# Optimization experiments

Hardware: AMD Instinct MI355X
Metric: run time of the kernel (lower is better)

The kernel has to match this reference:

```python
import jax, jax.numpy as jnp
import numpy as np

N, E, H, HEADS, L = 10000, 64000, 128, 8, 8
D = H // HEADS
CUTOFF = 5.0
EPS = 1e-5


def _xavier(key, shape):
    lim = float(np.sqrt(6.0 / (shape[0] + shape[1])))
    return jax.random.uniform(key, shape, minval=-lim, maxval=lim, dtype=jnp.float32)


def setup_inputs() -> dict:
    key = jax.random.key(0)
    ks = jax.random.split(key, 20)
    zeros = lambda *s: jnp.zeros(s, jnp.float32)
    return {
        "x": jax.random.normal(ks[0], (N, H), jnp.float32),
        "vec": 0.1 * jax.random.normal(ks[1], (N, L, H), jnp.float32),
        "f_ij": jax.random.normal(ks[2], (E, H), jnp.float32),
        "d_ij": jax.random.normal(ks[3], (E, L), jnp.float32),
        "r_ij": jax.random.uniform(ks[4], (E,), jnp.float32, 0.0, CUTOFF),
        "edge_index": jax.random.randint(ks[5], (2, E), 0, N),
        "ln_g": jnp.ones((H,), jnp.float32), "ln_b": zeros(H),
        "vln_w": jnp.ones((H,), jnp.float32),
        "W_vec": _xavier(ks[6], (H, 3 * H)),
        "W_q": _xavier(ks[7], (H, H)), "b_q": zeros(H),
        "W_k": _xavier(ks[8], (H, H)), "b_k": zeros(H),
        "W_v": _xavier(ks[9], (H, H)), "b_v": zeros(H),
        "W_dk": _xavier(ks[10], (H, H)), "b_dk": zeros(H),
        "W_dv": _xavier(ks[11], (H, H)), "b_dv": zeros(H),
        "W_s": _xavier(ks[12], (H, 2 * H)), "b_s": zeros(2 * H),
        "W_f": _xavier(ks[13], (H, H)), "b_f": zeros(H),
        "W_src": _xavier(ks[14], (H, H)),
        "W_trg": _xavier(ks[15], (H, H)),
        "W_o": _xavier(ks[16], (H, 3 * H)), "b_o": zeros(3 * H),
    }


def _layernorm(x, g, b):
    mu = jnp.mean(x, -1, keepdims=True)
    var = jnp.mean((x - mu) ** 2, -1, keepdims=True)
    return (x - mu) * jax.lax.rsqrt(var + EPS) * g + b


def _cutoff(r):
    # CosineCutoff: 0.5*(cos(pi*r/cutoff)+1) for r < cutoff
    return 0.5 * (jnp.cos(jnp.pi * r / CUTOFF) + 1.0) * (r < CUTOFF).astype(r.dtype)


def _vec_rejection(v, d):
    # v: [E, L, H], d: [E, L]; remove the component of v along d (per channel)
    proj = jnp.einsum("elh,el->eh", v, d)
    return v - proj[:, None, :] * d[:, :, None]


def reference(x, vec, f_ij, d_ij, r_ij, edge_index, ln_g, ln_b, vln_w, W_vec,
              W_q, b_q, W_k, b_k, W_v, b_v, W_dk, b_dk, W_dv, b_dv,
              W_s, b_s, W_f, b_f, W_src, W_trg, W_o, b_o):
    src, dst = edge_index[0], edge_index[1]  # j (source), i (target)
    x = _layernorm(x, ln_g, ln_b)
    vec = vec * vln_w  # VecLayerNorm with norm_type="none": identity norm * weight

    q = (x @ W_q + b_q).reshape(N, HEADS, D)
    k = (x @ W_k + b_k).reshape(N, HEADS, D)
    v = (x @ W_v + b_v).reshape(N, HEADS, D)
    dk = jax.nn.silu(f_ij @ W_dk + b_dk).reshape(E, HEADS, D)
    dv = jax.nn.silu(f_ij @ W_dv + b_dv).reshape(E, HEADS, D)

    vec1, vec2, vec3 = jnp.split(jnp.einsum("nlh,hk->nlk", vec, W_vec), 3, axis=-1)
    vec_dot = jnp.sum(vec1 * vec2, axis=1)  # [N, H]

    # ---- message (per edge) ----
    attn = jnp.sum(q[dst] * k[src] * dk, axis=-1)          # [E, HEADS]
    attn = jax.nn.silu(attn) * _cutoff(r_ij)[:, None]
    vm = (v[src] * dv * attn[:, :, None]).reshape(E, H)    # [E, H]
    s1, s2 = jnp.split(jax.nn.silu(vm @ W_s + b_s), 2, axis=-1)
    vec_m = vec[src] * s1[:, None, :] + s2[:, None, :] * d_ij[:, :, None]  # [E, L, H]

    # ---- aggregate (scatter-add to target nodes) ----
    x_agg = jax.ops.segment_sum(vm, dst, num_segments=N)       # [N, H]
    vec_agg = jax.ops.segment_sum(vec_m, dst, num_segments=N)  # [N, L, H]

    # ---- edge update ----
    w1 = _vec_rejection(jnp.einsum("elh,hk->elk", vec[dst], W_trg), d_ij)
    w2 = _vec_rejection(jnp.einsum("elh,hk->elk", vec[src], W_src), -d_ij)
    w_dot = jnp.sum(w1 * w2, axis=1)                       # [E, H]
    df_ij = jax.nn.silu(f_ij @ W_f + b_f) * w_dot

    # ---- node update ----
    o1, o2, o3 = jnp.split(x_agg @ W_o + b_o, 3, axis=-1)
    dx = vec_dot * o2 + o3
    dvec = vec3 * o1[:, None, :] + vec_agg
    return dx, dvec, df_ij
```

## Files before the change

### kernel.cpp

```cpp
#include <hip/hip_runtime.h>
#include <hip/hip_bf16.h>
#include <math.h>

#define N_NODES 10000
#define N_EDGES 64000
#define H 128
#define L 8
#define NL (N_NODES * L)

typedef __attribute__((ext_vector_type(4))) float f32x4;
typedef __attribute__((ext_vector_type(8))) __bf16 bf16x8;

__device__ __forceinline__ float silu_f(float x) { return x / (1.f + __expf(-x)); }

__global__ __launch_bounds__(256) void ln_kernel(const float* __restrict__ x,
                                                 const float* __restrict__ g,
                                                 const float* __restrict__ b,
                                                 __bf16* __restrict__ out, int n_nodes) {
  int wave = threadIdx.x >> 6;
  int lane = threadIdx.x & 63;
  int n = blockIdx.x * 4 + wave;
  if (n >= n_nodes) return;
  const float* xr = x + (size_t)n * H;
  float a0 = xr[lane], a1 = xr[lane + 64];
  float s = a0 + a1;
#pragma unroll
  for (int off = 32; off >= 1; off >>= 1) s += __shfl_xor(s, off, 64);
  float mu = s * (1.f / H);
  float d0 = a0 - mu, d1 = a1 - mu;
  float v = d0 * d0 + d1 * d1;
#pragma unroll
  for (int off = 32; off >= 1; off >>= 1) v += __shfl_xor(v, off, 64);
  float rstd = rsqrtf(v * (1.f / H) + 1e-5f);
  __bf16* orow = out + (size_t)n * H;
  orow[lane] = (__bf16)(d0 * rstd * g[lane] + b[lane]);
  orow[lane + 64] = (__bf16)(d1 * rstd * g[lane + 64] + b[lane + 64]);
}

__global__ __launch_bounds__(256) void vecw_kernel(const float* __restrict__ vec,
                                                   const float* __restrict__ w,
                                                   __bf16* __restrict__ out, size_t total8) {
  size_t i = (size_t)blockIdx.x * blockDim.x + threadIdx.x;
  size_t stride = (size_t)gridDim.x * blockDim.x;
  for (; i < total8; i += stride) {
    size_t base = i * 8;
    f32x4 a = *(const f32x4*)(vec + base);
    f32x4 b = *(const f32x4*)(vec + base + 4);
    int c = (int)(base & 127);
    bf16x8 h;
    h[0] = (__bf16)(a[0] * w[c + 0]); h[1] = (__bf16)(a[1] * w[c + 1]);
    h[2] = (__bf16)(a[2] * w[c + 2]); h[3] = (__bf16)(a[3] * w[c + 3]);
    h[4] = (__bf16)(b[0] * w[c + 4]); h[5] = (__bf16)(b[1] * w[c + 5]);
    h[6] = (__bf16)(b[2] * w[c + 6]); h[7] = (__bf16)(b[3] * w[c + 7]);
    *(bf16x8*)(out + base) = h;
  }
}

__global__ __launch_bounds__(256) void f2b_kernel(const float* __restrict__ in,
                                                  __bf16* __restrict__ out, size_t total8) {
  size_t i = (size_t)blockIdx.x * blockDim.x + threadIdx.x;
  size_t stride = (size_t)gridDim.x * blockDim.x;
  for (; i < total8; i += stride) {
    size_t base = i * 8;
    f32x4 a = *(const f32x4*)(in + base);
    f32x4 b = *(const f32x4*)(in + base + 4);
    bf16x8 h;
    h[0] = (__bf16)a[0]; h[1] = (__bf16)a[1]; h[2] = (__bf16)a[2]; h[3] = (__bf16)a[3];
    h[4] = (__bf16)b[0]; h[5] = (__bf16)b[1]; h[6] = (__bf16)b[2]; h[7] = (__bf16)b[3];
    *(bf16x8*)(out + base) = h;
  }
}

__global__ __launch_bounds__(256) void wconv_kernel(
    const float* __restrict__ Wvec, const float* __restrict__ Wq, const float* __restrict__ Wk,
    const float* __restrict__ Wv, const float* __restrict__ Wdk, const float* __restrict__ Wdv,
    const float* __restrict__ Ws, const float* __restrict__ Wtrg, const float* __restrict__ Wsrc,
    const float* __restrict__ Wf, const float* __restrict__ Wo,
    const float* __restrict__ bq, const float* __restrict__ bk, const float* __restrict__ bv,
    const float* __restrict__ bdk, const float* __restrict__ bdv, const float* __restrict__ bf,
    __bf16* __restrict__ Wt, float* __restrict__ bqkv, float* __restrict__ bfm) {
  int bid = blockIdx.x;
  int t = threadIdx.x;
  if (bid >= 256) {
    if (bid == 256) {
      if (t < 128) { bqkv[t] = bq[t]; bqkv[128 + t] = bk[t]; bqkv[256 + t] = bv[t]; }
    } else {
      if (t < 128) { bfm[t] = bdk[t]; bfm[128 + t] = bdv[t]; bfm[256 + t] = bf[t]; }
    }
    return;
  }
  int ct = bid >> 2, kt = bid & 3;
  int gc0 = ct * 32;
  const float* W; int ldw, sc0;
  if      (gc0 < 384)  { W = Wvec; ldw = 384; sc0 = gc0; }
  else if (gc0 < 512)  { W = Wtrg; ldw = 128; sc0 = gc0 - 384; }
  else if (gc0 < 640)  { W = Wsrc; ldw = 128; sc0 = gc0 - 512; }
  else if (gc0 < 768)  { W = Wq;   ldw = 128; sc0 = gc0 - 640; }
  else if (gc0 < 896)  { W = Wk;   ldw = 128; sc0 = gc0 - 768; }
  else if (gc0 < 1024) { W = Wv;   ldw = 128; sc0 = gc0 - 896; }
  else if (gc0 < 1152) { W = Wdk;  ldw = 128; sc0 = gc0 - 1024; }
  else if (gc0 < 1280) { W = Wdv;  ldw = 128; sc0 = gc0 - 1152; }
  else if (gc0 < 1408) { W = Wf;   ldw = 128; sc0 = gc0 - 1280; }
  else if (gc0 < 1664) { W = Ws;   ldw = 256; sc0 = gc0 - 1408; }
  else                 { W = Wo;   ldw = 384; sc0 = gc0 - 1664; }
  __shared__ float tile[32][33];
  int tx = t & 31, ty = t >> 5;
#pragma unroll
  for (int i = 0; i < 4; ++i)
    tile[ty + i * 8][tx] = W[(size_t)(kt * 32 + ty + i * 8) * ldw + sc0 + tx];
  __syncthreads();
#pragma unroll
  for (int i = 0; i < 4; ++i)
    Wt[(size_t)(gc0 + ty + i * 8) * 128 + kt * 32 + tx] = (__bf16)tile[tx][ty + i * 8];
}

__global__ __launch_bounds__(256, 2) void vdot_gemm(const __bf16* __restrict__ A,
                                                    const __bf16* __restrict__ Bt,
                                                    float* __restrict__ vdot) {
  __shared__ __bf16 As[128 * 128];
  const int tid = threadIdx.x;
  const int lane = tid & 63;
  const int wave = tid >> 6;
  const int wm = wave >> 1, wn = wave & 1;
  const int row0 = blockIdx.x * 128;

#pragma unroll
  for (int i = 0; i < 8; ++i) {
    int c = tid + i * 256;
    int row = c >> 4, k8 = c & 15;
    int k8s = k8 ^ (row & 7);
    const __bf16* src = A + (size_t)(row0 + row) * 128 + k8s * 8;
    __builtin_amdgcn_global_load_lds((const __attribute__((address_space(1))) void*)src,
                                     (__attribute__((address_space(3))) void*)(As + c * 8),
                                     16, 0, 0);
  }
  __syncthreads();

  f32x4 pacc[4][4], acc[4][4];
#pragma unroll
  for (int mi = 0; mi < 4; ++mi)
#pragma unroll
    for (int ni = 0; ni < 4; ++ni) {
      pacc[mi][ni] = f32x4{0.f, 0.f, 0.f, 0.f};
      acc[mi][ni] = f32x4{0.f, 0.f, 0.f, 0.f};
    }
#pragma unroll
  for (int ct = 0; ct < 2; ++ct) {
    const __bf16* Bbase =
        Bt + ((size_t)(ct * 128 + wn * 64 + (lane & 15)) << 7) + ((lane >> 4) << 3);
#pragma unroll
    for (int ks = 0; ks < 4; ++ks) {
      bf16x8 b[4];
#pragma unroll
      for (int ni = 0; ni < 4; ++ni) b[ni] = *(const bf16x8*)(Bbase + (ni << 11) + (ks << 5));
      bf16x8 a[4];
#pragma unroll
      for (int mi = 0; mi < 4; ++mi) {
        int row = wm * 64 + mi * 16 + (lane & 15);
        int byte = (row * 256 + ks * 64 + ((lane >> 4) << 4)) ^ ((row & 7) << 4);
        a[mi] = *(const bf16x8*)((const char*)As + byte);
      }
      if (ct == 0) {
#pragma unroll
        for (int mi = 0; mi < 4; ++mi)
#pragma unroll
          for (int ni = 0; ni < 4; ++ni)
            pacc[mi][ni] =
                __builtin_amdgcn_mfma_f32_16x16x32_bf16(a[mi], b[ni], pacc[mi][ni], 0, 0, 0);
      } else {
#pragma unroll
        for (int mi = 0; mi < 4; ++mi)
#pragma unroll
          for (int ni = 0; ni < 4; ++ni)
            acc[mi][ni] =
                __builtin_amdgcn_mfma_f32_16x16x32_bf16(a[mi], b[ni], acc[mi][ni], 0, 0, 0);
      }
    }
  }
#pragma unroll
  for (int mi = 0; mi < 4; ++mi) {
#pragma unroll
    for (int ni = 0; ni < 4; ++ni) {
      float sr = pacc[mi][ni][0] * acc[mi][ni][0] + pacc[mi][ni][1] * acc[mi][ni][1] +
                 pacc[mi][ni][2] * acc[mi][ni][2] + pacc[mi][ni][3] * acc[mi][ni][3];
      sr += __shfl_xor(sr, 16, 64);
      if ((lane & 16) == 0) {
        int node = (row0 >> 3) + wm * 8 + mi * 2 + (lane >> 5);
        int col = wn * 64 + ni * 16 + (lane & 15);
        vdot[(size_t)node * 128 + col] = sr;
      }
    }
  }
}

template <typename CT>
__global__ __launch_bounds__(256, 3) void gemm_v9(const __bf16* __restrict__ A,
                                                  const __bf16* __restrict__ Bt,
                                                  const float* __restrict__ bias,
                                                  CT* __restrict__ C, int M, int nx, int ny,
                                                  int ldc, int act) {
  __shared__ __bf16 As[128 * 128];
  __bf16* Cs = As;
  const int bid = blockIdx.x;
  const int xi = bid & 7;
  const int rem = bid >> 3;
  const int y = rem % ny;
  const int x = (rem / ny) * 8 + xi;
  if (x >= nx) return;
  const int tid = threadIdx.x;
  const int lane = tid & 63;
  const int wave = tid >> 6;
  const int wm = wave >> 1, wn = wave & 1;
  const int row0 = x * 128;

#pragma unroll
  for (int i = 0; i < 8; ++i) {
    int c = tid + i * 256;
    int row = c >> 4, k8 = c & 15;
    int k8s = k8 ^ (row & 7);
    const __bf16* src = A + (size_t)(row0 + row) * 128 + k8s * 8;
    __builtin_amdgcn_global_load_lds((const __attribute__((address_space(1))) void*)src,
                                     (__attribute__((address_space(3))) void*)(As + c * 8),
                                     16, 0, 0);
  }
  __syncthreads();

  const __bf16* Bbase =
      Bt + ((size_t)(y * 128 + wn * 64 + (lane & 15)) << 7) + ((lane >> 4) << 3);
  bf16x8 b[4][4];
#pragma unroll
  for (int ks = 0; ks < 4; ++ks)
#pragma unroll
    for (int ni = 0; ni < 4; ++ni) b[ks][ni] = *(const bf16x8*)(Bbase + (ni << 11) + (ks << 5));

  f32x4 acc[4][4];
#pragma unroll
  for (int mi = 0; mi < 4; ++mi)
#pragma unroll
    for (int ni = 0; ni < 4; ++ni) acc[mi][ni] = f32x4{0.f, 0.f, 0.f, 0.f};

#pragma unroll
  for (int ks = 0; ks < 4; ++ks) {
    bf16x8 a[4];
#pragma unroll
    for (int mi = 0; mi < 4; ++mi) {
      int row = wm * 64 + mi * 16 + (lane & 15);
      int byte = (row * 256 + ks * 64 + ((lane >> 4) << 4)) ^ ((row & 7) << 4);
      a[mi] = *(const bf16x8*)((const char*)As + byte);
    }
#pragma unroll
    for (int mi = 0; mi < 4; ++mi)
#pragma unroll
      for (int ni = 0; ni < 4; ++ni)
        acc[mi][ni] =
            __builtin_amdgcn_mfma_f32_16x16x32_bf16(a[mi], b[ks][ni], acc[mi][ni], 0, 0, 0);
  }

  const int cstore = y * 128;
  if constexpr (sizeof(CT) == 2) {
#pragma unroll
    for (int p = 0; p < 2; ++p) {
      __syncthreads();
      int rl = (wm << 5) | ((lane >> 4) << 2);
#pragma unroll
      for (int q = 0; q < 2; ++q) {
        int mi = 2 * p + q;
#pragma unroll
        for (int ni = 0; ni < 4; ++ni) {
          int col = wn * 64 + ni * 16 + (lane & 15);
          float bv = bias ? bias[cstore + col] : 0.f;
#pragma unroll
          for (int r = 0; r < 4; ++r) {
            float xv = acc[mi][ni][r] + bv;
            if (act) xv = silu_f(xv);
            Cs[(rl + q * 16 + r) * 136 + col] = (__bf16)xv;
          }
        }
      }
      __syncthreads();
#pragma unroll
      for (int rr = 0; rr < 4; ++rr) {
        int row = (tid >> 4) + rr * 16;
        int chunk = tid & 15;
        bf16x8 v = *(const bf16x8*)(Cs + row * 136 + chunk * 8);
        int grow = row0 + (row >> 5) * 64 + (2 * p + ((row >> 4) & 1)) * 16 + (row & 15);
        if (grow < M)
          *(bf16x8*)(C + (size_t)grow * ldc + cstore + chunk * 8) = v;
      }
    }
  } else {
#pragma unroll
    for (int mi = 0; mi < 4; ++mi) {
      int rbase = row0 + wm * 64 + mi * 16 + ((lane >> 4) << 2);
#pragma unroll
      for (int ni = 0; ni < 4; ++ni) {
        int gcol = cstore + wn * 64 + ni * 16 + (lane & 15);
        float bv = bias ? bias[cstore + wn * 64 + ni * 16 + (lane & 15)] : 0.f;
#pragma unroll
        for (int r = 0; r < 4; ++r) {
          int grow = rbase + r;
          if (grow < M) {
            float xv = acc[mi][ni][r] + bv;
            if (act) xv = silu_f(xv);
            C[(size_t)grow * ldc + gcol] = (CT)xv;
          }
        }
      }
    }
  }
}

static inline int swz_grid(int nx, int ny) { return ((nx + 7) / 8) * ny * 8; }

__global__ __launch_bounds__(256) void msg_kernel(const __bf16* __restrict__ qkv,
                                                  const __bf16* __restrict__ fm,
                                                  const float* __restrict__ r_ij,
                                                  const int* __restrict__ ei,
                                                  const int* __restrict__ elist,
                                                  __bf16* __restrict__ vm) {
  int p = blockIdx.x * 2 + (threadIdx.x >> 7);
  int h = threadIdx.x & 127;
  int e = elist[p];
  int src = ei[e], dst = ei[N_EDGES + e];
  float qv = (float)qkv[(size_t)dst * 384 + h];
  float kv = (float)qkv[(size_t)src * 384 + 128 + h];
  float vv = (float)qkv[(size_t)src * 384 + 256 + h];
  float t = qv * kv * (float)fm[(size_t)e * 384 + h];
#pragma unroll
  for (int off = 8; off >= 1; off >>= 1) t += __shfl_xor(t, off, 16);
  float r = r_ij[e];
  float cut = 0.5f * (__cosf(0.6283185307f * r) + 1.f);
  cut = (r < 5.f) ? cut : 0.f;
  float attn = silu_f(t) * cut;
  vm[(size_t)e * H + h] = (__bf16)(vv * (float)fm[(size_t)e * 384 + 128 + h] * attn);
}

__global__ __launch_bounds__(256) void hist_kernel(const int* __restrict__ ei,
                                                   int* __restrict__ cnt) {
  int e = blockIdx.x * 256 + threadIdx.x;
  if (e < N_EDGES) atomicAdd(&cnt[ei[N_EDGES + e]], 1);
}

__global__ __launch_bounds__(1024) void scan_kernel(const int* __restrict__ cnt,
                                                    int* __restrict__ rowptr) {
  __shared__ int wsum[16];
  int t = threadIdx.x;
  int base = t * 10;
  int local[10];
  int s = 0;
#pragma unroll
  for (int i = 0; i < 10; ++i) {
    int v = (base + i < N_NODES) ? cnt[base + i] : 0;
    local[i] = s;
    s += v;
  }
  int lane = t & 63, wave = t >> 6;
  int inc = s;
#pragma unroll
  for (int off = 1; off < 64; off <<= 1) {
    int u = __shfl_up(inc, off, 64);
    if (lane >= off) inc += u;
  }
  if (lane == 63) wsum[wave] = inc;
  __syncthreads();
  if (t == 0) {
    int acc = 0;
#pragma unroll
    for (int w = 0; w < 16; ++w) { int v = wsum[w]; wsum[w] = acc; acc += v; }
  }
  __syncthreads();
  int excl = inc - s + wsum[wave];
#pragma unroll
  for (int i = 0; i < 10; ++i)
    if (base + i <= N_NODES) rowptr[base + i] = excl + local[i];
}

__global__ __launch_bounds__(256) void fill_kernel(const int* __restrict__ ei,
                                                   const int* __restrict__ rowptr,
                                                   int* __restrict__ cursor,
                                                   int* __restrict__ elist) {
  int e = blockIdx.x * 256 + threadIdx.x;
  if (e < N_EDGES) {
    int d = ei[N_EDGES + e];
    int p = atomicAdd(&cursor[d], 1);
    elist[rowptr[d] + p] = e;
  }
}

__global__ __launch_bounds__(256) void node_kernel(const __bf16* __restrict__ vm,
                                                   const __bf16* __restrict__ s,
                                                   const __bf16* __restrict__ vecw,
                                                   const __bf16* __restrict__ big,
                                                   const __bf16* __restrict__ fm,
                                                   const float* __restrict__ d_ij,
                                                   const int* __restrict__ ei,
                                                   const int* __restrict__ rowptr,
                                                   const int* __restrict__ elist,
                                                   __bf16* __restrict__ x_agg,
                                                   float* __restrict__ dvec,
                                                   float* __restrict__ df) {
  int n = blockIdx.x * 2 + (threadIdx.x >> 7);
  int h = threadIdx.x & 127;
  if (n >= N_NODES) return;
  int beg = rowptr[n], end = rowptr[n + 1];

  float vt[L];
  const __bf16* trow = big + (size_t)n * 8 * 384 + 128 + h;
#pragma unroll
  for (int l = 0; l < L; l++) vt[l] = (float)trow[l * 384];

  float ax = 0.f;
  float av[L] = {};
  for (int p = beg; p < end; ++p) {
    int e = elist[p];
    int src = ei[e];
    const float* dd = d_ij + (size_t)e * L;
    float d[L], sd2 = 0.f;
#pragma unroll
    for (int l = 0; l < L; l++) {
      d[l] = dd[l];
      sd2 += d[l] * d[l];
    }
    ax += (float)vm[(size_t)e * H + h];
    float s1 = (float)s[(size_t)e * 256 + h];
    float s2 = (float)s[(size_t)e * 256 + 128 + h];
    const __bf16* vrow = vecw + (size_t)src * L * H + h;
    const __bf16* brow = big + (size_t)src * 8 * 384 + 256 + h;
    float dot = 0.f, p1 = 0.f, p2 = 0.f;
#pragma unroll
    for (int l = 0; l < L; l++) {
      float vw = (float)vrow[l * H];
      av[l] += vw * s1 + s2 * d[l];
      float bb = (float)brow[l * 384];
      dot += vt[l] * bb;
      p1 += vt[l] * d[l];
      p2 += bb * d[l];
    }
    float wdot = dot - p1 * p2 * (2.f - sd2);
    df[(size_t)e * H + h] = (float)fm[(size_t)e * 384 + 256 + h] * wdot;
  }
  x_agg[(size_t)n * H + h] = (__bf16)ax;
  float* drow = dvec + (size_t)n * L * H + h;
#pragma unroll
  for (int l = 0; l < L; l++) drow[l * H] = av[l];
}

__global__ __launch_bounds__(256) void final_kernel(const float* __restrict__ o,
                                                    const float* __restrict__ vdot,
                                                    const __bf16* __restrict__ big,
                                                    float* __restrict__ dx,
                                                    float* __restrict__ dvec, int n_nodes) {
  int n = blockIdx.x * 2 + (threadIdx.x >> 7);
  int h = threadIdx.x & 127;
  if (n >= n_nodes) return;
  float o1 = o[(size_t)n * 384 + h];
  float o2 = o[(size_t)n * 384 + 128 + h];
  float o3 = o[(size_t)n * 384 + 256 + h];
  dx[(size_t)n * H + h] = vdot[(size_t)n * H + h] * o2 + o3;
  float* drow = dvec + (size_t)n * L * H + h;
  const __bf16* v3 = big + (size_t)n * 8 * 384 + h;
#pragma unroll
  for (int l = 0; l < L; l++) drow[l * H] += (float)v3[l * 384] * o1;
}

extern "C" void kernel_launch(void* const* d_in, const int* in_sizes, int n_in, void* d_out,
                              int out_size, void* d_ws, size_t ws_size, hipStream_t stream) {
  const float* x = (const float*)d_in[0];
  const float* vec = (const float*)d_in[1];
  const float* f_ij = (const float*)d_in[2];
  const float* d_ij = (const float*)d_in[3];
  const float* r_ij = (const float*)d_in[4];
  const int* ei = (const int*)d_in[5];
  const float* ln_g = (const float*)d_in[6];
  const float* ln_b = (const float*)d_in[7];
  const float* vln_w = (const float*)d_in[8];
  const float* W_vec = (const float*)d_in[9];
  const float* W_q = (const float*)d_in[10];
  const float* b_q = (const float*)d_in[11];
  const float* W_k = (const float*)d_in[12];
  const float* b_k = (const float*)d_in[13];
  const float* W_v = (const float*)d_in[14];
  const float* b_v = (const float*)d_in[15];
  const float* W_dk = (const float*)d_in[16];
  const float* b_dk = (const float*)d_in[17];
  const float* W_dv = (const float*)d_in[18];
  const float* b_dv = (const float*)d_in[19];
  const float* W_s = (const float*)d_in[20];
  const float* b_s = (const float*)d_in[21];
  const float* W_f = (const float*)d_in[22];
  const float* b_f = (const float*)d_in[23];
  const float* W_src = (const float*)d_in[24];
  const float* W_trg = (const float*)d_in[25];
  const float* W_o = (const float*)d_in[26];
  const float* b_o = (const float*)d_in[27];

  float* out = (float*)d_out;
  float* dx = out;
  float* dvec = out + (size_t)N_NODES * H;
  float* df = dvec + (size_t)N_NODES * L * H;

  float* ws = (float*)d_ws;
  __bf16* vecw = (__bf16*)ws;
  __bf16* big = (__bf16*)(ws + 5120000);
  __bf16* fm = (__bf16*)(ws + 20480000);
  __bf16* vm = (__bf16*)(ws + 32768000);
  __bf16* s_buf = (__bf16*)(ws + 36864000);
  __bf16* qkv = (__bf16*)(ws + 45056000);
  __bf16* xln = (__bf16*)(ws + 48896000);
  __bf16* xagg = (__bf16*)(ws + 49536000);
  float* vdot = ws + 50176000;
  __bf16* Wt = (__bf16*)(ws + 51456000);
  float* bqkv = ws + 51456000 + 131072;
  float* bfm = bqkv + 384;
  int* rowptr = (int*)(bfm + 384);
  int* elist = rowptr + 10001;
  int* cnt = elist + 64000;
  int* cursor = cnt + 10000;
  __bf16* fijb = (__bf16*)(ws + 51800000);

  float* o_buf = ws + 45056000;

  dim3 b256(256);

  hipMemsetAsync(cnt, 0, N_NODES * sizeof(int), stream);
  hipMemsetAsync(cursor, 0, N_NODES * sizeof(int), stream);
  hist_kernel<<<dim3((N_EDGES + 255) / 256), b256, 0, stream>>>(ei, cnt);
  scan_kernel<<<dim3(1), dim3(1024), 0, stream>>>(cnt, rowptr);
  fill_kernel<<<dim3((N_EDGES + 255) / 256), b256, 0, stream>>>(ei, rowptr, cursor, elist);

  wconv_kernel<<<dim3(258), b256, 0, stream>>>(W_vec, W_q, W_k, W_v, W_dk, W_dv, W_s, W_trg,
                                               W_src, W_f, W_o, b_q, b_k, b_v, b_dk, b_dv, b_f,
                                               Wt, bqkv, bfm);
  f2b_kernel<<<dim3(2048), b256, 0, stream>>>(f_ij, fijb, (size_t)N_EDGES * H / 8);
  ln_kernel<<<dim3((N_NODES + 3) / 4), b256, 0, stream>>>(x, ln_g, ln_b, xln, N_NODES);
  vecw_kernel<<<dim3(2048), b256, 0, stream>>>(vec, vln_w, vecw, (size_t)NL * H / 8);
  vdot_gemm<<<dim3(625), b256, 0, stream>>>(vecw, Wt, vdot);
  gemm_v9<__bf16><<<dim3(swz_grid(625, 3)), b256, 0, stream>>>(
      vecw, Wt + (size_t)256 * 128, nullptr, big, NL, 625, 3, 384, 0);
  gemm_v9<__bf16><<<dim3(swz_grid(79, 3)), b256, 0, stream>>>(
      xln, Wt + (size_t)640 * 128, bqkv, qkv, N_NODES, 79, 3, 384, 0);
  gemm_v9<__bf16><<<dim3(swz_grid(500, 3)), b256, 0, stream>>>(
      fijb, Wt + (size_t)1024 * 128, bfm, fm, N_EDGES, 500, 3, 384, 1);
  msg_kernel<<<dim3(N_EDGES / 2), b256, 0, stream>>>(qkv, fm, r_ij, ei, elist, vm);
  gemm_v9<__bf16><<<dim3(swz_grid(500, 2)), b256, 0, stream>>>(
      vm, Wt + (size_t)1408 * 128, b_s, s_buf, N_EDGES, 500, 2, 256, 1);
  node_kernel<<<dim3(N_NODES / 2), b256, 0, stream>>>(vm, s_buf, vecw, big, fm, d_ij, ei,
                                                      rowptr, elist, xagg, dvec, df);
  gemm_v9<float><<<dim3(swz_grid(79, 3)), b256, 0, stream>>>(
      xagg, Wt + (size_t)1664 * 128, b_o, o_buf, N_NODES, 79, 3, 384, 0);
  final_kernel<<<dim3(5000), b256, 0, stream>>>(o_buf, vdot, big, dx, dvec, N_NODES);
}
```

Measured before the change: 321.5 us.

## Store per-edge tensors in dst-sorted order and transpose vec projections for node gathers

f_ij is now gathered and converted to bf16 in destination-sorted edge order, so fm, vm and s are laid out contiguously by sorted position and the node kernel reads them sequentially instead of through scattered edge ids. A dedicated GEMM for the vec projection writes vec3 in plain layout and the W_trg/W_src outputs transposed as [node][h][l], so each thread reads one 16-byte vector instead of eight strided loads. The costs are a gather in the conversion kernel and an LDS transpose in the GEMM epilogue.

```diff
diff --git a/kernel.cpp b/kernel.cpp
--- a/kernel.cpp
+++ b/kernel.cpp
@@ -10,6 +10,7 @@
 
 typedef __attribute__((ext_vector_type(4))) float f32x4;
 typedef __attribute__((ext_vector_type(8))) __bf16 bf16x8;
+typedef __attribute__((ext_vector_type(4))) __bf16 bf16x4;
 
 __device__ __forceinline__ float silu_f(float x) { return x / (1.f + __expf(-x)); }
 
@@ -56,19 +57,16 @@
   }
 }
 
-__global__ __launch_bounds__(256) void f2b_kernel(const float* __restrict__ in,
-                                                  __bf16* __restrict__ out, size_t total8) {
-  size_t i = (size_t)blockIdx.x * blockDim.x + threadIdx.x;
-  size_t stride = (size_t)gridDim.x * blockDim.x;
-  for (; i < total8; i += stride) {
-    size_t base = i * 8;
-    f32x4 a = *(const f32x4*)(in + base);
-    f32x4 b = *(const f32x4*)(in + base + 4);
-    bf16x8 h;
-    h[0] = (__bf16)a[0]; h[1] = (__bf16)a[1]; h[2] = (__bf16)a[2]; h[3] = (__bf16)a[3];
-    h[4] = (__bf16)b[0]; h[5] = (__bf16)b[1]; h[6] = (__bf16)b[2]; h[7] = (__bf16)b[3];
-    *(bf16x8*)(out + base) = h;
-  }
+__global__ __launch_bounds__(256) void gatherf2b_kernel(const float* __restrict__ in,
+                                                        const int* __restrict__ elist,
+                                                        __bf16* __restrict__ out) {
+  int p = blockIdx.x * 8 + (threadIdx.x >> 5);
+  int c = (threadIdx.x & 31) * 4;
+  int e = elist[p];
+  f32x4 a = *(const f32x4*)(in + (size_t)e * 128 + c);
+  bf16x4 h;
+  h[0] = (__bf16)a[0]; h[1] = (__bf16)a[1]; h[2] = (__bf16)a[2]; h[3] = (__bf16)a[3];
+  *(bf16x4*)(out + (size_t)p * 128 + c) = h;
 }
 
 __global__ __launch_bounds__(256) void wconv_kernel(
@@ -310,6 +308,112 @@
   }
 }
 
+__global__ __launch_bounds__(256, 3) void gemm_big(const __bf16* __restrict__ A,
+                                                   const __bf16* __restrict__ Bt,
+                                                   __bf16* __restrict__ vec3,
+                                                   __bf16* __restrict__ vtT,
+                                                   __bf16* __restrict__ vsT, int nx) {
+  __shared__ __bf16 As[128 * 128];
+  __bf16* Cs = As;
+  const int bid = blockIdx.x;
+  const int xi = bid & 7;
+  const int rem = bid >> 3;
+  const int y = rem % 3;
+  const int x = (rem / 3) * 8 + xi;
+  if (x >= nx) return;
+  const int tid = threadIdx.x;
+  const int lane = tid & 63;
+  const int wave = tid >> 6;
+  const int wm = wave >> 1, wn = wave & 1;
+  const int row0 = x * 128;
+
+#pragma unroll
+  for (int i = 0; i < 8; ++i) {
+    int c = tid + i * 256;
+    int row = c >> 4, k8 = c & 15;
+    int k8s = k8 ^ (row & 7);
+    const __bf16* src = A + (size_t)(row0 + row) * 128 + k8s * 8;
+    __builtin_amdgcn_global_load_lds((const __attribute__((address_space(1))) void*)src,
+                                     (__attribute__((address_space(3))) void*)(As + c * 8),
+                                     16, 0, 0);
+  }
+  __syncthreads();
+
+  const __bf16* Bbase =
+      Bt + ((size_t)(y * 128 + wn * 64 + (lane & 15)) << 7) + ((lane >> 4) << 3);
+  bf16x8 b[4][4];
+#pragma unroll
+  for (int ks = 0; ks < 4; ++ks)
+#pragma unroll
+    for (int ni = 0; ni < 4; ++ni) b[ks][ni] = *(const bf16x8*)(Bbase + (ni << 11) + (ks << 5));
+
+  f32x4 acc[4][4];
+#pragma unroll
+  for (int mi = 0; mi < 4; ++mi)
+#pragma unroll
+    for (int ni = 0; ni < 4; ++ni) acc[mi][ni] = f32x4{0.f, 0.f, 0.f, 0.f};
+
+#pragma unroll
+  for (int ks = 0; ks < 4; ++ks) {
+    bf16x8 a[4];
+#pragma unroll
+    for (int mi = 0; mi < 4; ++mi) {
+      int row = wm * 64 + mi * 16 + (lane & 15);
+      int byte = (row * 256 + ks * 64 + ((lane >> 4) << 4)) ^ ((row & 7) << 4);
+      a[mi] = *(const bf16x8*)((const char*)As + byte);
+    }
+#pragma unroll
+    for (int mi = 0; mi < 4; ++mi)
+#pragma unroll
+      for (int ni = 0; ni < 4; ++ni)
+        acc[mi][ni] =
+            __builtin_amdgcn_mfma_f32_16x16x32_bf16(a[mi], b[ks][ni], acc[mi][ni], 0, 0, 0);
+  }
+
+  __bf16* T = (y == 1) ? vtT : vsT;
+#pragma unroll
+  for (int p = 0; p < 2; ++p) {
+    __syncthreads();
+    int rl = (wm << 5) | ((lane >> 4) << 2);
+#pragma unroll
+    for (int q = 0; q < 2; ++q) {
+      int mi = 2 * p + q;
+#pragma unroll
+      for (int ni = 0; ni < 4; ++ni) {
+        int col = wn * 64 + ni * 16 + (lane & 15);
+#pragma unroll
+        for (int r = 0; r < 4; ++r)
+          Cs[(rl + q * 16 + r) * 136 + col] = (__bf16)acc[mi][ni][r];
+      }
+    }
+    __syncthreads();
+    if (y == 0) {
+#pragma unroll
+      for (int rr = 0; rr < 4; ++rr) {
+        int row = (tid >> 4) + rr * 16;
+        int chunk = tid & 15;
+        bf16x8 v = *(const bf16x8*)(Cs + row * 136 + chunk * 8);
+        int grow = row0 + (row >> 5) * 64 + (2 * p + ((row >> 4) & 1)) * 16 + (row & 15);
+        *(bf16x8*)(vec3 + (size_t)grow * 128 + chunk * 8) = v;
+      }
+    } else {
+#pragma unroll
+      for (int j = 0; j < 4; ++j) {
+        int idx = tid + 256 * j;
+        int node_idx = idx >> 7;
+        int h = idx & 127;
+        int wmm = node_idx >> 2, qq = (node_idx >> 1) & 1, w = node_idx & 1;
+        int base = wmm * 32 + qq * 16 + w * 8;
+        bf16x8 v;
+#pragma unroll
+        for (int l = 0; l < 8; ++l) v[l] = Cs[(base + l) * 136 + h];
+        int g = (row0 >> 3) + wmm * 8 + (2 * p + qq) * 2 + w;
+        *(bf16x8*)(T + (size_t)g * 1024 + h * 8) = v;
+      }
+    }
+  }
+}
+
 static inline int swz_grid(int nx, int ny) { return ((nx + 7) / 8) * ny * 8; }
 
 __global__ __launch_bounds__(256) void msg_kernel(const __bf16* __restrict__ qkv,
@@ -325,14 +429,14 @@
   float qv = (float)qkv[(size_t)dst * 384 + h];
   float kv = (float)qkv[(size_t)src * 384 + 128 + h];
   float vv = (float)qkv[(size_t)src * 384 + 256 + h];
-  float t = qv * kv * (float)fm[(size_t)e * 384 + h];
+  float t = qv * kv * (float)fm[(size_t)p * 384 + h];
 #pragma unroll
   for (int off = 8; off >= 1; off >>= 1) t += __shfl_xor(t, off, 16);
   float r = r_ij[e];
   float cut = 0.5f * (__cosf(0.6283185307f * r) + 1.f);
   cut = (r < 5.f) ? cut : 0.f;
   float attn = silu_f(t) * cut;
-  vm[(size_t)e * H + h] = (__bf16)(vv * (float)fm[(size_t)e * 384 + 128 + h] * attn);
+  vm[(size_t)p * H + h] = (__bf16)(vv * (float)fm[(size_t)p * 384 + 128 + h] * attn);
 }
 
 __global__ __launch_bounds__(256) void hist_kernel(const int* __restrict__ ei,
@@ -390,7 +494,8 @@
 __global__ __launch_bounds__(256) void node_kernel(const __bf16* __restrict__ vm,
                                                    const __bf16* __restrict__ s,
                                                    const __bf16* __restrict__ vecw,
-                                                   const __bf16* __restrict__ big,
+                                                   const __bf16* __restrict__ vtT,
+                                                   const __bf16* __restrict__ vsT,
                                                    const __bf16* __restrict__ fm,
                                                    const float* __restrict__ d_ij,
                                                    const int* __restrict__ ei,
@@ -404,10 +509,10 @@
   if (n >= N_NODES) return;
   int beg = rowptr[n], end = rowptr[n + 1];
 
+  bf16x8 vt8 = *(const bf16x8*)(vtT + (size_t)n * 1024 + h * 8);
   float vt[L];
-  const __bf16* trow = big + (size_t)n * 8 * 384 + 128 + h;
-#pragma unroll
-  for (int l = 0; l < L; l++) vt[l] = (float)trow[l * 384];
+#pragma unroll
+  for (int l = 0; l < L; l++) vt[l] = (float)vt8[l];
 
   float ax = 0.f;
   float av[L] = {};
@@ -421,23 +526,23 @@
       d[l] = dd[l];
       sd2 += d[l] * d[l];
     }
-    ax += (float)vm[(size_t)e * H + h];
-    float s1 = (float)s[(size_t)e * 256 + h];
-    float s2 = (float)s[(size_t)e * 256 + 128 + h];
+    ax += (float)vm[(size_t)p * H + h];
+    float s1 = (float)s[(size_t)p * 256 + h];
+    float s2 = (float)s[(size_t)p * 256 + 128 + h];
+    bf16x8 vs8 = *(const bf16x8*)(vsT + (size_t)src * 1024 + h * 8);
     const __bf16* vrow = vecw + (size_t)src * L * H + h;
-    const __bf16* brow = big + (size_t)src * 8 * 384 + 256 + h;
     float dot = 0.f, p1 = 0.f, p2 = 0.f;
 #pragma unroll
     for (int l = 0; l < L; l++) {
       float vw = (float)vrow[l * H];
       av[l] += vw * s1 + s2 * d[l];
-      float bb = (float)brow[l * 384];
+      float bb = (float)vs8[l];
       dot += vt[l] * bb;
       p1 += vt[l] * d[l];
       p2 += bb * d[l];
     }
     float wdot = dot - p1 * p2 * (2.f - sd2);
-    df[(size_t)e * H + h] = (float)fm[(size_t)e * 384 + 256 + h] * wdot;
+    df[(size_t)e * H + h] = (float)fm[(size_t)p * 384 + 256 + h] * wdot;
   }
   x_agg[(size_t)n * H + h] = (__bf16)ax;
   float* drow = dvec + (size_t)n * L * H + h;
@@ -447,7 +552,7 @@
 
 __global__ __launch_bounds__(256) void final_kernel(const float* __restrict__ o,
                                                     const float* __restrict__ vdot,
-                                                    const __bf16* __restrict__ big,
+                                                    const __bf16* __restrict__ vec3,
                                                     float* __restrict__ dx,
                                                     float* __restrict__ dvec, int n_nodes) {
   int n = blockIdx.x * 2 + (threadIdx.x >> 7);
@@ -458,9 +563,9 @@
   float o3 = o[(size_t)n * 384 + 256 + h];
   dx[(size_t)n * H + h] = vdot[(size_t)n * H + h] * o2 + o3;
   float* drow = dvec + (size_t)n * L * H + h;
-  const __bf16* v3 = big + (size_t)n * 8 * 384 + h;
-#pragma unroll
-  for (int l = 0; l < L; l++) drow[l * H] += (float)v3[l * 384] * o1;
+  const __bf16* v3 = vec3 + (size_t)n * 1024 + h;
+#pragma unroll
+  for (int l = 0; l < L; l++) drow[l * H] += (float)v3[l * 128] * o1;
 }
 
 extern "C" void kernel_launch(void* const* d_in, const int* in_sizes, int n_in, void* d_out,
@@ -501,7 +606,9 @@
 
   float* ws = (float*)d_ws;
   __bf16* vecw = (__bf16*)ws;
-  __bf16* big = (__bf16*)(ws + 5120000);
+  __bf16* vec3 = (__bf16*)(ws + 5120000);
+  __bf16* vtT = (__bf16*)(ws + 10240000);
+  __bf16* vsT = (__bf16*)(ws + 15360000);
   __bf16* fm = (__bf16*)(ws + 20480000);
   __bf16* vm = (__bf16*)(ws + 32768000);
   __bf16* s_buf = (__bf16*)(ws + 36864000);
@@ -531,12 +638,12 @@
   wconv_kernel<<<dim3(258), b256, 0, stream>>>(W_vec, W_q, W_k, W_v, W_dk, W_dv, W_s, W_trg,
                                                W_src, W_f, W_o, b_q, b_k, b_v, b_dk, b_dv, b_f,
                                                Wt, bqkv, bfm);
-  f2b_kernel<<<dim3(2048), b256, 0, stream>>>(f_ij, fijb, (size_t)N_EDGES * H / 8);
+  gatherf2b_kernel<<<dim3(N_EDGES / 8), b256, 0, stream>>>(f_ij, elist, fijb);
   ln_kernel<<<dim3((N_NODES + 3) / 4), b256, 0, stream>>>(x, ln_g, ln_b, xln, N_NODES);
   vecw_kernel<<<dim3(2048), b256, 0, stream>>>(vec, vln_w, vecw, (size_t)NL * H / 8);
   vdot_gemm<<<dim3(625), b256, 0, stream>>>(vecw, Wt, vdot);
-  gemm_v9<__bf16><<<dim3(swz_grid(625, 3)), b256, 0, stream>>>(
-      vecw, Wt + (size_t)256 * 128, nullptr, big, NL, 625, 3, 384, 0);
+  gemm_big<<<dim3(swz_grid(625, 3)), b256, 0, stream>>>(vecw, Wt + (size_t)256 * 128, vec3,
+                                                        vtT, vsT, 625);
   gemm_v9<__bf16><<<dim3(swz_grid(79, 3)), b256, 0, stream>>>(
       xln, Wt + (size_t)640 * 128, bqkv, qkv, N_NODES, 79, 3, 384, 0);
   gemm_v9<__bf16><<<dim3(swz_grid(500, 3)), b256, 0, stream>>>(
@@ -544,9 +651,9 @@
   msg_kernel<<<dim3(N_EDGES / 2), b256, 0, stream>>>(qkv, fm, r_ij, ei, elist, vm);
   gemm_v9<__bf16><<<dim3(swz_grid(500, 2)), b256, 0, stream>>>(
       vm, Wt + (size_t)1408 * 128, b_s, s_buf, N_EDGES, 500, 2, 256, 1);
-  node_kernel<<<dim3(N_NODES / 2), b256, 0, stream>>>(vm, s_buf, vecw, big, fm, d_ij, ei,
+  node_kernel<<<dim3(N_NODES / 2), b256, 0, stream>>>(vm, s_buf, vecw, vtT, vsT, fm, d_ij, ei,
                                                       rowptr, elist, xagg, dvec, df);
   gemm_v9<float><<<dim3(swz_grid(79, 3)), b256, 0, stream>>>(
       xagg, Wt + (size_t)1664 * 128, b_o, o_buf, N_NODES, 79, 3, 384, 0);
-  final_kernel<<<dim3(5000), b256, 0, stream>>>(o_buf, vdot, big, dx, dvec, N_NODES);
-}
+  final_kernel<<<dim3(5000), b256, 0, stream>>>(o_buf, vdot, vec3, dx, dvec, N_NODES);
+}
```

New measurement: 309.0 us. 3.9% less time.
